# Kernel tuning notes

Measured on AMD Instinct MI355X. Metric: run time of the kernel, lower is better.

Reference implementation:

```python
import jax, jax.numpy as jnp
import numpy as np

N_HEAD = 16


def setup_inputs() -> dict:
    key = jax.random.key(0)
    ks = jax.random.split(key, 9)
    B, T, C = 4, 2048, 1024
    s = 1.0 / np.sqrt(C)
    x = jax.random.normal(ks[0], (B, T, C), dtype=jnp.float32)
    Wq = jax.random.normal(ks[1], (C, C), dtype=jnp.float32) * s
    bq = jnp.zeros((C,), dtype=jnp.float32)
    Wk = jax.random.normal(ks[2], (C, C), dtype=jnp.float32) * s
    bk = jnp.zeros((C,), dtype=jnp.float32)
    Wv = jax.random.normal(ks[3], (C, C), dtype=jnp.float32) * s
    bv = jnp.zeros((C,), dtype=jnp.float32)
    Wp = jax.random.normal(ks[4], (C, C), dtype=jnp.float32) * s
    bp = jnp.zeros((C,), dtype=jnp.float32)
    return {"x": x, "Wq": Wq, "bq": bq, "Wk": Wk, "bk": bk,
            "Wv": Wv, "bv": bv, "Wp": Wp, "bp": bp}


def reference(x, Wq, bq, Wk, bk, Wv, bv, Wp, bp):
    B, T, C = x.shape
    H = N_HEAD
    D = C // H
    # QKV projections, then split heads: [B, T, C] -> [B, H, T, D]
    def split_heads(t):
        return t.reshape(B, T, H, D).transpose(0, 2, 1, 3)
    q = split_heads(x @ Wq.T + bq)
    k = split_heads(x @ Wk.T + bk)
    v = split_heads(x @ Wv.T + bv)
    # NOTE: original code applies NO causal mask despite the class name.
    att = jnp.einsum('bhtd,bhsd->bhts', q, k) * (1.0 / jnp.sqrt(jnp.float32(D)))
    att = jax.nn.softmax(att, axis=-1)
    y = jnp.einsum('bhts,bhsd->bhtd', att, v)  # [B, H, T, D]
    y = y.transpose(0, 2, 1, 3).reshape(B, T, C)
    return y @ Wp.T + bp
```

## Files before the change

kernel.cpp:

```cpp
#include <hip/hip_runtime.h>
#include <hip/hip_bf16.h>

typedef float  f32x4   __attribute__((ext_vector_type(4)));
typedef short  bf16x8  __attribute__((ext_vector_type(8)));

__device__ __forceinline__ ushort f2b(float f) {
  union { float f; unsigned u; } x; x.f = f;
  unsigned r = x.u + 0x7fffu + ((x.u >> 16) & 1u);
  return (ushort)(r >> 16);
}

__device__ __forceinline__ unsigned pk2(float lo, float hi) {
  __hip_bfloat162 t = __float22bfloat162_rn(make_float2(lo, hi));
  union { __hip_bfloat162 b; unsigned u; } c; c.b = t; return c.u;
}

__device__ __forceinline__ f32x4 fzero() {
  f32x4 z; z[0] = 0.f; z[1] = 0.f; z[2] = 0.f; z[3] = 0.f; return z;
}

__device__ __forceinline__ void gld_lds16(const ushort* g, ushort* l) {
  __builtin_amdgcn_global_load_lds(g, l, 16, 0, 0);
}

__device__ __forceinline__ int vperm_s(int j64) {
  return (j64 & 0x23) | ((j64 & 0x0C) << 1) | ((j64 & 0x10) >> 2);
}

__global__ __launch_bounds__(256) void f2bf_kernel(const float* __restrict__ in,
                                                   ushort* __restrict__ out, int n4) {
  int idx = blockIdx.x * 256 + threadIdx.x;
  int stride = gridDim.x * 256;
  for (int i = idx; i < n4; i += stride) {
    float4 v = reinterpret_cast<const float4*>(in)[i];
    ushort4 o;
    o.x = f2b(v.x); o.y = f2b(v.y); o.z = f2b(v.z); o.w = f2b(v.w);
    reinterpret_cast<ushort4*>(out)[i] = o;
  }
}

__global__ __launch_bounds__(256) void f2bf_w4(
    const float* __restrict__ w0, const float* __restrict__ w1,
    const float* __restrict__ w2, const float* __restrict__ w3,
    ushort* __restrict__ out, int n4) {
  const float* src = (blockIdx.y == 0) ? w0 : (blockIdx.y == 1) ? w1
                   : (blockIdx.y == 2) ? w2 : w3;
  ushort* dst = out + (size_t)blockIdx.y * (size_t)n4 * 4;
  int idx = blockIdx.x * 256 + threadIdx.x;
  int stride = gridDim.x * 256;
  for (int i = idx; i < n4; i += stride) {
    float4 v = reinterpret_cast<const float4*>(src)[i];
    ushort4 o;
    o.x = f2b(v.x); o.y = f2b(v.y); o.z = f2b(v.z); o.w = f2b(v.w);
    reinterpret_cast<ushort4*>(dst)[i] = o;
  }
}

__global__ __launch_bounds__(256) void gemm_bt_n64(
    const ushort* __restrict__ A, const ushort* __restrict__ B,
    const float* __restrict__ bias, float* __restrict__ Cf,
    int M, int N, int K) {
  __shared__ ushort As[128 * 32];
  __shared__ ushort Bs[64 * 32];
  const int tid = threadIdx.x, lane = tid & 63, wave = tid >> 6;
  const int wr = (wave >> 1) << 6, wc = (wave & 1) << 5;
  const int fr = lane & 15, fk8 = (lane >> 4) << 3;

  const int orig = blockIdx.y * 16 + blockIdx.x;
  const int swz  = (orig & 7) * 128 + (orig >> 3);
  const int bx = swz & 15, by = swz >> 4;

  const size_t rowA = (size_t)by * 128;
  const size_t rowB = (size_t)bx * 64;
  const ushort* Ag = A + rowA * K;
  const ushort* Bg = B + rowB * K;

  const int c0 = tid, c1 = tid + 256;
  const size_t a0 = (size_t)(c0 >> 2) * K + (size_t)((c0 & 3) << 3);
  const size_t a1 = (size_t)(c1 >> 2) * K + (size_t)((c1 & 3) << 3);

  f32x4 acc[4][2];
#pragma unroll
  for (int m = 0; m < 4; ++m)
#pragma unroll
    for (int n = 0; n < 2; ++n) acc[m][n] = fzero();

  for (int k0 = 0; k0 < K; k0 += 32) {
    __syncthreads();
    gld_lds16(Ag + a0 + k0, &As[wave * 512]);
    gld_lds16(Ag + a1 + k0, &As[2048 + wave * 512]);
    gld_lds16(Bg + a0 + k0, &Bs[wave * 512]);
    asm volatile("s_waitcnt vmcnt(0)" ::: "memory");
    __syncthreads();

    bf16x8 af[4], bfv[2];
#pragma unroll
    for (int m = 0; m < 4; ++m)
      af[m] = *reinterpret_cast<const bf16x8*>(&As[(wr + m * 16 + fr) * 32 + fk8]);
#pragma unroll
    for (int n = 0; n < 2; ++n)
      bfv[n] = *reinterpret_cast<const bf16x8*>(&Bs[(wc + n * 16 + fr) * 32 + fk8]);
#pragma unroll
    for (int m = 0; m < 4; ++m)
#pragma unroll
      for (int n = 0; n < 2; ++n)
        acc[m][n] = __builtin_amdgcn_mfma_f32_16x16x32_bf16(af[m], bfv[n], acc[m][n], 0, 0, 0);
  }

  const int orow = (lane >> 4) << 2;
#pragma unroll
  for (int m = 0; m < 4; ++m) {
#pragma unroll
    for (int n = 0; n < 2; ++n) {
      size_t gc = rowB + wc + n * 16 + fr;
      float bv = bias[gc];
#pragma unroll
      for (int r = 0; r < 4; ++r) {
        size_t gr = rowA + wr + m * 16 + orow + r;
        Cf[gr * N + gc] = acc[m][n][r] + bv;
      }
    }
  }
}

__global__ __launch_bounds__(256) void gemm_qkv(
    const ushort* __restrict__ A, const ushort* __restrict__ Bw,
    const float* __restrict__ bq, const float* __restrict__ bk, const float* __restrict__ bv,
    ushort* __restrict__ Qb, ushort* __restrict__ Kb, ushort* __restrict__ VbT,
    float qscale) {
  __shared__ ushort As[128 * 32];
  __shared__ ushort Bs[128 * 32];
  const int tid = threadIdx.x, lane = tid & 63, wave = tid >> 6;
  const int wr = (wave >> 1) << 6, wc = (wave & 1) << 6;
  const int fr = lane & 15, fk8 = (lane >> 4) << 3;
  const int K = 1024;

  const int orig = blockIdx.y * 24 + blockIdx.x;
  const int swz  = (orig & 7) * 192 + (orig >> 3);
  const int bx = swz % 24, by = swz / 24;

  const size_t rowA = (size_t)by * 128;
  const size_t rowB = (size_t)bx * 128;
  const ushort* Ag = A + rowA * K;
  const ushort* Bg = Bw + rowB * K;

  const int c0 = tid, c1 = tid + 256;
  const size_t a0 = (size_t)(c0 >> 2) * K + (size_t)((c0 & 3) << 3);
  const size_t a1 = (size_t)(c1 >> 2) * K + (size_t)((c1 & 3) << 3);

  f32x4 acc[4][4];
#pragma unroll
  for (int m = 0; m < 4; ++m)
#pragma unroll
    for (int n = 0; n < 4; ++n) acc[m][n] = fzero();

  for (int k0 = 0; k0 < K; k0 += 32) {
    __syncthreads();
    gld_lds16(Ag + a0 + k0, &As[wave * 512]);
    gld_lds16(Ag + a1 + k0, &As[2048 + wave * 512]);
    gld_lds16(Bg + a0 + k0, &Bs[wave * 512]);
    gld_lds16(Bg + a1 + k0, &Bs[2048 + wave * 512]);
    asm volatile("s_waitcnt vmcnt(0)" ::: "memory");
    __syncthreads();

    bf16x8 af[4], bfv[4];
#pragma unroll
    for (int m = 0; m < 4; ++m)
      af[m] = *reinterpret_cast<const bf16x8*>(&As[(wr + m * 16 + fr) * 32 + fk8]);
#pragma unroll
    for (int n = 0; n < 4; ++n)
      bfv[n] = *reinterpret_cast<const bf16x8*>(&Bs[(wc + n * 16 + fr) * 32 + fk8]);
#pragma unroll
    for (int m = 0; m < 4; ++m)
#pragma unroll
      for (int n = 0; n < 4; ++n)
        acc[m][n] = __builtin_amdgcn_mfma_f32_16x16x32_bf16(af[m], bfv[n], acc[m][n], 0, 0, 0);
  }

  const int stripe  = bx >> 3;
  const int colbase = (bx & 7) * 128;
  const int orow = (lane >> 4) << 2;
#pragma unroll
  for (int m = 0; m < 4; ++m) {
#pragma unroll
    for (int n = 0; n < 4; ++n) {
      const int gcl = colbase + wc + n * 16 + fr;
      if (stripe == 0) {
        const float bb_ = bq[gcl];
#pragma unroll
        for (int r = 0; r < 4; ++r) {
          size_t gr = rowA + wr + m * 16 + orow + r;
          Qb[gr * 1024 + gcl] = f2b((acc[m][n][r] + bb_) * qscale);
        }
      } else if (stripe == 1) {
        const float bb_ = bk[gcl];
#pragma unroll
        for (int r = 0; r < 4; ++r) {
          size_t gr = rowA + wr + m * 16 + orow + r;
          Kb[gr * 1024 + gcl] = f2b(acc[m][n][r] + bb_);
        }
      } else {
        const float bb_ = bv[gcl];
        int tt0 = (int)rowA + wr + m * 16 + orow;
        int b = tt0 >> 11, t = tt0 & 2047;
        size_t idx0 = (size_t)b * 2097152 + (size_t)gcl * 2048
                    + (size_t)((t & ~63) + vperm_s(t & 63));
        ushort4 o;
        o.x = f2b(acc[m][n][0] + bb_);
        o.y = f2b(acc[m][n][1] + bb_);
        o.z = f2b(acc[m][n][2] + bb_);
        o.w = f2b(acc[m][n][3] + bb_);
        *reinterpret_cast<ushort4*>(&VbT[idx0]) = o;
      }
    }
  }
}

__global__ __launch_bounds__(512, 4) void attn_kernel(
    const ushort* __restrict__ Qb, const ushort* __restrict__ Kb,
    const ushort* __restrict__ VbT, ushort* __restrict__ Yb) {
  __shared__ ushort lds[16384];
  const int tid = threadIdx.x, lane = tid & 63, wave = tid >> 6;
  const int fr = lane & 15, g = lane >> 4, fk8 = g << 3;
  const int bb = blockIdx.y >> 4, hh = blockIdx.y & 15;
  const size_t rowbase = (size_t)bb * 2048;
  const int cbase = hh * 64;
  const ushort* Kg  = Kb  + rowbase * 1024 + cbase;
  const ushort* VgT = VbT + (size_t)bb * 2097152 + (size_t)cbase * 2048;

  const int qrow = blockIdx.x * 128 + wave * 16 + fr;
  const ushort* qptr = &Qb[(rowbase + qrow) * 1024 + cbase];
  const bf16x8 qf0 = *reinterpret_cast<const bf16x8*>(qptr + fk8);
  const bf16x8 qf1 = *reinterpret_cast<const bf16x8*>(qptr + 32 + fk8);

  const int rS = tid >> 3;
  const int wS = (tid & 7) ^ (rS & 7);
  const ushort* sKp = Kg  + (size_t)rS * 1024 + (wS << 3);
  const ushort* sVp = VgT + (size_t)rS * 2048 + (wS << 3);
  const int wofs = wave * 512;

  const int e0 = (g ^ (fr & 7)) << 3;
  const int e1 = ((4 + g) ^ (fr & 7)) << 3;
  const ushort* lpA = &lds[fr * 64 + e0];
  const ushort* lpB = &lds[fr * 64 + e1];

  f32x4 yacc[4];
#pragma unroll
  for (int nb = 0; nb < 4; ++nb) yacc[nb] = fzero();
  f32x4 psum4 = fzero();

#define LD8(P) (*reinterpret_cast<const bf16x8*>(P))
#define MF16(A, B, C) __builtin_amdgcn_mfma_f32_16x16x32_bf16(A, B, C, 0, 0, 0)

  gld_lds16(sKp, &lds[wofs]);  gld_lds16(sVp, &lds[8192 + wofs]);  sKp += 65536; sVp += 64;
  asm volatile("s_waitcnt vmcnt(0)" ::: "memory");
  __builtin_amdgcn_s_barrier();
  __builtin_amdgcn_sched_barrier(0);

#define TILE(BUF, DOPF) do {                                                     \
    if (DOPF) {    \
      gld_lds16(sKp, &lds[((BUF) ^ 1) * 4096 + wofs]);                           \
      gld_lds16(sVp, &lds[8192 + ((BUF) ^ 1) * 4096 + wofs]);                    \
      sKp += 65536; sVp += 64;                                                   \
    }                                                                            \
    f32x4 sT[4];                                                                 \
    _Pragma("unroll")                                                            \
    for (int jb = 0; jb < 4; ++jb) {                                             \
      bf16x8 kf0 = LD8(lpA + (BUF) * 4096 + jb * 1024);                          \
      bf16x8 kf1 = LD8(lpB + (BUF) * 4096 + jb * 1024);                          \
      f32x4 z = fzero();                                                         \
      __builtin_amdgcn_s_setprio(1);                                             \
      z = MF16(kf0, qf0, z);                                                     \
      z = MF16(kf1, qf1, z);                                                     \
      __builtin_amdgcn_s_setprio(0);                                             \
      sT[jb] = z;                                                                \
    }                                                                            \
    _Pragma("unroll")                                                            \
    for (int jb = 0; jb < 4; ++jb)                                               \
      _Pragma("unroll")                                                          \
      for (int r = 0; r < 4; ++r) sT[jb][r] = __builtin_exp2f(sT[jb][r]);        \
    _Pragma("unroll")                                                            \
    for (int r = 0; r < 4; ++r)                                                  \
      psum4[r] += (sT[0][r] + sT[1][r]) + (sT[2][r] + sT[3][r]);                 \
    union { bf16x8 v; unsigned u[4]; } pa0, pa1;                                 \
    pa0.u[0] = pk2(sT[0][0], sT[0][1]); pa0.u[1] = pk2(sT[0][2], sT[0][3]);      \
    pa0.u[2] = pk2(sT[1][0], sT[1][1]); pa0.u[3] = pk2(sT[1][2], sT[1][3]);      \
    pa1.u[0] = pk2(sT[2][0], sT[2][1]); pa1.u[1] = pk2(sT[2][2], sT[2][3]);      \
    pa1.u[2] = pk2(sT[3][0], sT[3][1]); pa1.u[3] = pk2(sT[3][2], sT[3][3]);      \
    _Pragma("unroll")                                                            \
    for (int nb = 0; nb < 4; ++nb) {                                             \
      bf16x8 vf0 = LD8(lpA + 8192 + (BUF) * 4096 + nb * 1024);                   \
      bf16x8 vf1 = LD8(lpB + 8192 + (BUF) * 4096 + nb * 1024);                   \
      __builtin_amdgcn_s_setprio(1);                                             \
      yacc[nb] = MF16(vf0, pa0.v, yacc[nb]);                                     \
      yacc[nb] = MF16(vf1, pa1.v, yacc[nb]);                                     \
      __builtin_amdgcn_s_setprio(0);                                             \
    }                                                                            \
    asm volatile("s_waitcnt vmcnt(0)" ::: "memory");                             \
    __builtin_amdgcn_s_barrier();                                                \
    __builtin_amdgcn_sched_barrier(0);                                           \
  } while (0)

  for (int tb = 0; tb < 30; tb += 2) {
    TILE(0, 1);
    TILE(1, 1);
  }
  TILE(0, 1);
  TILE(1, 0);
#undef TILE
#undef MF16
#undef LD8

  float psum = (psum4[0] + psum4[1]) + (psum4[2] + psum4[3]);
  psum += __shfl_xor(psum, 16);
  psum += __shfl_xor(psum, 32);
  const float linv = 1.0f / psum;
  ushort* yrow = &Yb[(rowbase + qrow) * 1024 + cbase];
#pragma unroll
  for (int nb = 0; nb < 4; ++nb) {
    ushort4 o;
    o.x = f2b(yacc[nb][0] * linv);
    o.y = f2b(yacc[nb][1] * linv);
    o.z = f2b(yacc[nb][2] * linv);
    o.w = f2b(yacc[nb][3] * linv);
    *reinterpret_cast<ushort4*>(yrow + nb * 16 + (g << 2)) = o;
  }
}

extern "C" void kernel_launch(void* const* d_in, const int* in_sizes, int n_in,
                              void* d_out, int out_size, void* d_ws, size_t ws_size,
                              hipStream_t stream) {
  const float* x  = (const float*)d_in[0];
  const float* Wq = (const float*)d_in[1];
  const float* bq = (const float*)d_in[2];
  const float* Wk = (const float*)d_in[3];
  const float* bk = (const float*)d_in[4];
  const float* Wv = (const float*)d_in[5];
  const float* bv = (const float*)d_in[6];
  const float* Wp = (const float*)d_in[7];
  const float* bp = (const float*)d_in[8];
  float* out = (float*)d_out;

  const int M = 8192, C = 1024;
  const size_t MC = (size_t)M * C, CC = (size_t)C * C;
  const size_t need = (MC * 5 + CC * 4) * sizeof(ushort);
  if (ws_size < need) return;

  ushort* xb  = (ushort*)d_ws;
  ushort* wqb = xb + MC;
  ushort* wpb = wqb + 3 * CC;
  ushort* Qb  = wpb + CC;
  ushort* Kb  = Qb + MC;
  ushort* VbT = Kb + MC;
  ushort* Yb  = VbT + MC;

  f2bf_kernel<<<2048, 256, 0, stream>>>(x, xb, (int)(MC / 4));
  f2bf_w4<<<dim3(256, 4), 256, 0, stream>>>(Wq, Wk, Wv, Wp, wqb, (int)(CC / 4));

  const float QSCALE = 0.18033688011112042f;
  gemm_qkv<<<dim3(24, 64), 256, 0, stream>>>(xb, wqb, bq, bk, bv, Qb, Kb, VbT, QSCALE);

  attn_kernel<<<dim3(16, 64), 512, 0, stream>>>(Qb, Kb, VbT, Yb);

  gemm_bt_n64<<<dim3(16, 64), 256, 0, stream>>>(Yb, wpb, bp, out, M, C, C);
}
```

Before: 232.6 us.

## Triple-buffer LDS in projection GEMMs to overlap global loads with MFMA

Replaces the single-buffered load-wait-compute loop in the output-projection and QKV GEMMs with a three-stage LDS ring. Each step prefetches the tile two steps ahead through global_load_lds and waits only for the older in-flight loads via partial vmcnt counts, with one barrier per step instead of two. This is meant to hide global-memory latency behind MFMA work. It triples LDS use per block, which can lower occupancy, and it hardcodes K=1024 (32 k-steps), so the loop count is fixed regardless of the K argument.

Result: faster. 225.6 us, median of 3 (-3.0%).

```diff
diff --git a/kernel.cpp b/kernel.cpp
--- a/kernel.cpp
+++ b/kernel.cpp
@@ -60,8 +60,7 @@
     const ushort* __restrict__ A, const ushort* __restrict__ B,
     const float* __restrict__ bias, float* __restrict__ Cf,
     int M, int N, int K) {
-  __shared__ ushort As[128 * 32];
-  __shared__ ushort Bs[64 * 32];
+  __shared__ ushort lds[18432];
   const int tid = threadIdx.x, lane = tid & 63, wave = tid >> 6;
   const int wr = (wave >> 1) << 6, wc = (wave & 1) << 5;
   const int fr = lane & 15, fk8 = (lane >> 4) << 3;
@@ -78,6 +77,10 @@
   const int c0 = tid, c1 = tid + 256;
   const size_t a0 = (size_t)(c0 >> 2) * K + (size_t)((c0 & 3) << 3);
   const size_t a1 = (size_t)(c1 >> 2) * K + (size_t)((c1 & 3) << 3);
+  const ushort* sA0 = Ag + a0;
+  const ushort* sA1 = Ag + a1;
+  const ushort* sB0 = Bg + a0;
+  const int wofs = wave * 512;
 
   f32x4 acc[4][2];
 #pragma unroll
@@ -85,27 +88,50 @@
 #pragma unroll
     for (int n = 0; n < 2; ++n) acc[m][n] = fzero();
 
-  for (int k0 = 0; k0 < K; k0 += 32) {
-    __syncthreads();
-    gld_lds16(Ag + a0 + k0, &As[wave * 512]);
-    gld_lds16(Ag + a1 + k0, &As[2048 + wave * 512]);
-    gld_lds16(Bg + a0 + k0, &Bs[wave * 512]);
-    asm volatile("s_waitcnt vmcnt(0)" ::: "memory");
-    __syncthreads();
-
-    bf16x8 af[4], bfv[2];
-#pragma unroll
-    for (int m = 0; m < 4; ++m)
-      af[m] = *reinterpret_cast<const bf16x8*>(&As[(wr + m * 16 + fr) * 32 + fk8]);
-#pragma unroll
-    for (int n = 0; n < 2; ++n)
-      bfv[n] = *reinterpret_cast<const bf16x8*>(&Bs[(wc + n * 16 + fr) * 32 + fk8]);
-#pragma unroll
-    for (int m = 0; m < 4; ++m)
-#pragma unroll
-      for (int n = 0; n < 2; ++n)
-        acc[m][n] = __builtin_amdgcn_mfma_f32_16x16x32_bf16(af[m], bfv[n], acc[m][n], 0, 0, 0);
-  }
+#define LD8(P) (*reinterpret_cast<const bf16x8*>(P))
+#define MF16(A_, B_, C_) __builtin_amdgcn_mfma_f32_16x16x32_bf16(A_, B_, C_, 0, 0, 0)
+#define STAGEP(BUF) do {                                                         \
+    gld_lds16(sA0, &lds[(BUF) * 4096 + wofs]);                                   \
+    gld_lds16(sA1, &lds[(BUF) * 4096 + 2048 + wofs]);                            \
+    gld_lds16(sB0, &lds[12288 + (BUF) * 2048 + wofs]);                           \
+    sA0 += 32; sA1 += 32; sB0 += 32;                                             \
+  } while (0)
+#define KSTEPP(BUF, DOPF, VMASM) do {                                            \
+    if (DOPF) STAGEP(((BUF) + 2) % 3);                                           \
+    bf16x8 af[4], bfv[2];                                                        \
+    _Pragma("unroll")                                                            \
+    for (int m = 0; m < 4; ++m)                                                  \
+      af[m] = LD8(&lds[(BUF) * 4096 + (wr + m * 16 + fr) * 32 + fk8]);           \
+    _Pragma("unroll")                                                            \
+    for (int n = 0; n < 2; ++n)                                                  \
+      bfv[n] = LD8(&lds[12288 + (BUF) * 2048 + (wc + n * 16 + fr) * 32 + fk8]);  \
+    _Pragma("unroll")                                                            \
+    for (int m = 0; m < 4; ++m)                                                  \
+      _Pragma("unroll")                                                          \
+      for (int n = 0; n < 2; ++n)                                                \
+        acc[m][n] = MF16(af[m], bfv[n], acc[m][n]);                              \
+    asm volatile(VMASM ::: "memory");                                            \
+    __builtin_amdgcn_s_barrier();                                                \
+    __builtin_amdgcn_sched_barrier(0);                                           \
+  } while (0)
+
+  STAGEP(0);
+  STAGEP(1);
+  asm volatile("s_waitcnt vmcnt(3)" ::: "memory");
+  __builtin_amdgcn_s_barrier();
+  __builtin_amdgcn_sched_barrier(0);
+
+  for (int tb = 0; tb < 30; tb += 3) {
+    KSTEPP(0, 1, "s_waitcnt vmcnt(3)");
+    KSTEPP(1, 1, "s_waitcnt vmcnt(3)");
+    KSTEPP(2, 1, "s_waitcnt vmcnt(3)");
+  }
+  KSTEPP(0, 0, "s_waitcnt vmcnt(0)");
+  KSTEPP(1, 0, "");
+#undef KSTEPP
+#undef STAGEP
+#undef MF16
+#undef LD8
 
   const int orow = (lane >> 4) << 2;
 #pragma unroll
@@ -128,8 +154,7 @@
     const float* __restrict__ bq, const float* __restrict__ bk, const float* __restrict__ bv,
     ushort* __restrict__ Qb, ushort* __restrict__ Kb, ushort* __restrict__ VbT,
     float qscale) {
-  __shared__ ushort As[128 * 32];
-  __shared__ ushort Bs[128 * 32];
+  __shared__ ushort lds[24576];
   const int tid = threadIdx.x, lane = tid & 63, wave = tid >> 6;
   const int wr = (wave >> 1) << 6, wc = (wave & 1) << 6;
   const int fr = lane & 15, fk8 = (lane >> 4) << 3;
@@ -147,6 +172,11 @@
   const int c0 = tid, c1 = tid + 256;
   const size_t a0 = (size_t)(c0 >> 2) * K + (size_t)((c0 & 3) << 3);
   const size_t a1 = (size_t)(c1 >> 2) * K + (size_t)((c1 & 3) << 3);
+  const ushort* sA0 = Ag + a0;
+  const ushort* sA1 = Ag + a1;
+  const ushort* sB0 = Bg + a0;
+  const ushort* sB1 = Bg + a1;
+  const int wofs = wave * 512;
 
   f32x4 acc[4][4];
 #pragma unroll
@@ -154,28 +184,51 @@
 #pragma unroll
     for (int n = 0; n < 4; ++n) acc[m][n] = fzero();
 
-  for (int k0 = 0; k0 < K; k0 += 32) {
-    __syncthreads();
-    gld_lds16(Ag + a0 + k0, &As[wave * 512]);
-    gld_lds16(Ag + a1 + k0, &As[2048 + wave * 512]);
-    gld_lds16(Bg + a0 + k0, &Bs[wave * 512]);
-    gld_lds16(Bg + a1 + k0, &Bs[2048 + wave * 512]);
-    asm volatile("s_waitcnt vmcnt(0)" ::: "memory");
-    __syncthreads();
-
-    bf16x8 af[4], bfv[4];
-#pragma unroll
-    for (int m = 0; m < 4; ++m)
-      af[m] = *reinterpret_cast<const bf16x8*>(&As[(wr + m * 16 + fr) * 32 + fk8]);
-#pragma unroll
-    for (int n = 0; n < 4; ++n)
-      bfv[n] = *reinterpret_cast<const bf16x8*>(&Bs[(wc + n * 16 + fr) * 32 + fk8]);
-#pragma unroll
-    for (int m = 0; m < 4; ++m)
-#pragma unroll
-      for (int n = 0; n < 4; ++n)
-        acc[m][n] = __builtin_amdgcn_mfma_f32_16x16x32_bf16(af[m], bfv[n], acc[m][n], 0, 0, 0);
-  }
+#define LD8(P) (*reinterpret_cast<const bf16x8*>(P))
+#define MF16(A_, B_, C_) __builtin_amdgcn_mfma_f32_16x16x32_bf16(A_, B_, C_, 0, 0, 0)
+#define STAGEQ(BUF) do {                                                         \
+    gld_lds16(sA0, &lds[(BUF) * 4096 + wofs]);                                   \
+    gld_lds16(sA1, &lds[(BUF) * 4096 + 2048 + wofs]);                            \
+    gld_lds16(sB0, &lds[12288 + (BUF) * 4096 + wofs]);                           \
+    gld_lds16(sB1, &lds[12288 + (BUF) * 4096 + 2048 + wofs]);                    \
+    sA0 += 32; sA1 += 32; sB0 += 32; sB1 += 32;                                  \
+  } while (0)
+#define KSTEPQ(BUF, DOPF, VMASM) do {                                            \
+    if (DOPF) STAGEQ(((BUF) + 2) % 3);                                           \
+    bf16x8 af[4], bfv[4];                                                        \
+    _Pragma("unroll")                                                            \
+    for (int m = 0; m < 4; ++m)                                                  \
+      af[m] = LD8(&lds[(BUF) * 4096 + (wr + m * 16 + fr) * 32 + fk8]);           \
+    _Pragma("unroll")                                                            \
+    for (int n = 0; n < 4; ++n)                                                  \
+      bfv[n] = LD8(&lds[12288 + (BUF) * 4096 + (wc + n * 16 + fr) * 32 + fk8]);  \
+    _Pragma("unroll")                                                            \
+    for (int m = 0; m < 4; ++m)                                                  \
+      _Pragma("unroll")                                                          \
+      for (int n = 0; n < 4; ++n)                                                \
+        acc[m][n] = MF16(af[m], bfv[n], acc[m][n]);                              \
+    asm volatile(VMASM ::: "memory");                                            \
+    __builtin_amdgcn_s_barrier();                                                \
+    __builtin_amdgcn_sched_barrier(0);                                           \
+  } while (0)
+
+  STAGEQ(0);
+  STAGEQ(1);
+  asm volatile("s_waitcnt vmcnt(4)" ::: "memory");
+  __builtin_amdgcn_s_barrier();
+  __builtin_amdgcn_sched_barrier(0);
+
+  for (int tb = 0; tb < 30; tb += 3) {
+    KSTEPQ(0, 1, "s_waitcnt vmcnt(4)");
+    KSTEPQ(1, 1, "s_waitcnt vmcnt(4)");
+    KSTEPQ(2, 1, "s_waitcnt vmcnt(4)");
+  }
+  KSTEPQ(0, 0, "s_waitcnt vmcnt(0)");
+  KSTEPQ(1, 0, "");
+#undef KSTEPQ
+#undef STAGEQ
+#undef MF16
+#undef LD8
 
   const int stripe  = bx >> 3;
   const int colbase = (bx & 7) * 128;
```
